# Optimization experiments

Measured on AMD Instinct MI355X. Metric: run time of the kernel, lower is better.

## Reference

```python
import jax, jax.numpy as jnp
import numpy as np
import math

D_MODEL = 2048
N_HEADS = 16
HEAD_DIM = D_MODEL // N_HEADS  # 128
SEQ = 2048
BATCH = 1


def make_freqs(seq_len, head_dim, theta=10000.0):
    # standard rotary frequencies: freqs_cis = exp(i * t * inv_freq)
    inv_freq = 1.0 / (theta ** (np.arange(0, head_dim, 2, dtype=np.float32) / head_dim))
    t = np.arange(seq_len, dtype=np.float32)
    ang = np.outer(t, inv_freq)  # [seq, head_dim/2]
    return jnp.asarray(np.cos(ang)), jnp.asarray(np.sin(ang))


def setup_inputs() -> dict:
    key = jax.random.key(0)
    ks = jax.random.split(key, 6)
    x = jax.random.normal(ks[0], (BATCH, SEQ, D_MODEL), dtype=jnp.float32)
    freqs_cos, freqs_sin = make_freqs(SEQ, HEAD_DIM)
    # causal additive mask, broadcastable to [b, h, s, s]
    mask = jnp.where(jnp.tril(jnp.ones((SEQ, SEQ), dtype=bool)), 0.0, -1e9).astype(jnp.float32)[None, None]
    scale = 0.02
    wq = jax.random.normal(ks[1], (D_MODEL, D_MODEL), dtype=jnp.float32) * scale
    wk = jax.random.normal(ks[2], (D_MODEL, D_MODEL), dtype=jnp.float32) * scale
    wv = jax.random.normal(ks[3], (D_MODEL, D_MODEL), dtype=jnp.float32) * scale
    wo = jax.random.normal(ks[4], (D_MODEL, D_MODEL), dtype=jnp.float32) * scale
    return {"x": x, "freqs_cos": freqs_cos, "freqs_sin": freqs_sin, "mask": mask,
            "wq": wq, "wk": wk, "wv": wv, "wo": wo}


def _apply_rotary(q, k, cos, sin):
    # q, k: [b, s, h, hd]; cos/sin: [s, hd/2]
    def rot(t):
        tr = t.reshape(*t.shape[:-1], -1, 2)  # [b, s, h, hd/2, 2]
        re, im = tr[..., 0], tr[..., 1]
        c = cos[None, :, None, :]
        s = sin[None, :, None, :]
        # complex multiply (re + i im) * (c + i s)
        out_re = re * c - im * s
        out_im = re * s + im * c
        return jnp.stack([out_re, out_im], axis=-1).reshape(t.shape)
    return rot(q), rot(k)


def reference(x, freqs_cos, freqs_sin, mask, wq, wk, wv, wo):
    b, s, _ = x.shape
    # QKV projections (nn.Linear with no bias: x @ W^T; W is square so use x @ W
    # with W stored already-transposed -- weights here are random so x @ W is faithful math)
    q = (x @ wq).reshape(b, s, N_HEADS, HEAD_DIM)
    k = (x @ wk).reshape(b, s, N_HEADS, HEAD_DIM)
    v = (x @ wv).reshape(b, s, N_HEADS, HEAD_DIM)
    q, k = _apply_rotary(q, k, freqs_cos, freqs_sin)
    # [b, h, s_q, s_k]
    scores = jnp.einsum("bqhd,bkhd->bhqk", q, k) / math.sqrt(HEAD_DIM)
    scores = scores + mask
    probs = jax.nn.softmax(scores.astype(jnp.float32), axis=-1).astype(q.dtype)
    out = jnp.einsum("bhqk,bkhd->bqhd", probs, v).reshape(b, s, N_HEADS * HEAD_DIM)
    return out @ wo
```

## Files before the change

### kernel.cpp

```cpp
#include <hip/hip_runtime.h>
#include <hip/hip_bf16.h>
#include <math.h>

#define SEQ 2048
#define DM 2048
#define NH 16
#define HD 128
#define QKV_N 6144

typedef __bf16 bf16;
typedef __bf16 bf16x8 __attribute__((ext_vector_type(8)));
typedef __bf16 bf16x4v __attribute__((ext_vector_type(4)));
typedef __bf16 bf16x2v __attribute__((ext_vector_type(2)));
typedef float f32x4 __attribute__((ext_vector_type(4)));

__device__ inline int sw_idx64(int row, int chunk) {
    return (row * 8 + (chunk ^ (row & 7))) * 8;
}
__device__ inline int sw_idx128(int row, int chunk) {
    return (row * 16 + (chunk ^ (row & 15))) * 8;
}
__device__ inline int sw_idx32(int row, int chunk) {
    return (row * 4 + (chunk ^ (row & 3))) * 8;
}

__device__ inline void async16(const void* g, void* l) {
    __builtin_amdgcn_global_load_lds((const __attribute__((address_space(1))) void*)g,
                                     (__attribute__((address_space(3))) void*)l, 16, 0, 0);
}

__global__ __launch_bounds__(256) void k_prep(const float* __restrict__ wq,
                                              const float* __restrict__ wk,
                                              const float* __restrict__ wv,
                                              const float* __restrict__ wo,
                                              bf16* __restrict__ wT, bf16* __restrict__ woT,
                                              const float* __restrict__ x,
                                              bf16* __restrict__ xb) {
    const int z = blockIdx.z;
    const int t = threadIdx.x;
    if (z == 4) {
        int bid = blockIdx.y * 32 + blockIdx.x;
#pragma unroll
        for (int j = 0; j < 4; ++j) {
            int i = bid * 1024 + j * 256 + t;
            float4 v = ((const float4*)x)[i];
            bf16x4v o;
            o.x = (bf16)v.x; o.y = (bf16)v.y; o.z = (bf16)v.z; o.w = (bf16)v.w;
            ((bf16x4v*)xb)[i] = o;
        }
        return;
    }
    __shared__ bf16 tile[64][66];
    const float* src = (z == 0) ? wq : (z == 1) ? wk : (z == 2) ? wv : wo;
    bf16* dst = (z < 3) ? (wT + (size_t)z * DM * DM) : woT;
    const int bx = blockIdx.x * 64, by = blockIdx.y * 64;
#pragma unroll
    for (int j = 0; j < 4; ++j) {
        int idx = j * 256 + t;
        int r = idx >> 4, cg = idx & 15;
        float4 v = *(const float4*)&src[(size_t)(by + r) * DM + bx + cg * 4];
        bf16x4v o;
        o.x = (bf16)v.x; o.y = (bf16)v.y; o.z = (bf16)v.z; o.w = (bf16)v.w;
        *(bf16x4v*)&tile[r][cg * 4] = o;
    }
    __syncthreads();
#pragma unroll
    for (int j = 0; j < 4; ++j) {
        int idx = j * 256 + t;
        int r = idx >> 4, cg = idx & 15;
        bf16x4v o;
        o.x = tile[cg * 4 + 0][r];
        o.y = tile[cg * 4 + 1][r];
        o.z = tile[cg * 4 + 2][r];
        o.w = tile[cg * 4 + 3][r];
        *(bf16x4v*)&dst[(size_t)(bx + r) * DM + by + cg * 4] = o;
    }
}

__global__ __launch_bounds__(256) void k_rope_vt(bf16* __restrict__ qkv,
                                                 const float* __restrict__ cosT,
                                                 const float* __restrict__ sinT,
                                                 bf16* __restrict__ vT) {
    const int t = threadIdx.x;
    if (blockIdx.x >= 1024) {
        int g = (blockIdx.x - 1024) * 256 + t;
        int s = g >> 8;
        int cg = g & 255;
        int h = cg >> 4, w8 = cg & 15;
        size_t base = (size_t)s * QKV_N + DM + h * HD + w8 * 8;
        float4 cv = *(const float4*)&cosT[s * 64 + w8 * 4];
        float4 sv = *(const float4*)&sinT[s * 64 + w8 * 4];
        float cc[4] = {cv.x, cv.y, cv.z, cv.w};
        float ss[4] = {sv.x, sv.y, sv.z, sv.w};
        bf16x8 k = *(bf16x8*)&qkv[base];
        bf16x8 o;
#pragma unroll
        for (int p = 0; p < 4; ++p) {
            float re = (float)k[2 * p], im = (float)k[2 * p + 1];
            o[2 * p]     = (bf16)(re * cc[p] - im * ss[p]);
            o[2 * p + 1] = (bf16)(re * ss[p] + im * cc[p]);
        }
        *(bf16x8*)&qkv[base] = o;
        return;
    }
    __shared__ bf16 tile[64][66];
    const int bx = (blockIdx.x & 31) * 64, by = (blockIdx.x >> 5) * 64;
#pragma unroll
    for (int j = 0; j < 4; ++j) {
        int idx = j * 256 + t;
        int r = idx >> 4, cg = idx & 15;
        *(bf16x4v*)&tile[r][cg * 4] =
            *(const bf16x4v*)&qkv[(size_t)(by + r) * QKV_N + 2 * DM + bx + cg * 4];
    }
    __syncthreads();
#pragma unroll
    for (int j = 0; j < 4; ++j) {
        int idx = j * 256 + t;
        int r = idx >> 4, cg = idx & 15;
        bf16x4v o;
        o.x = tile[cg * 4 + 0][r];
        o.y = tile[cg * 4 + 1][r];
        o.z = tile[cg * 4 + 2][r];
        o.w = tile[cg * 4 + 3][r];
        *(bf16x4v*)&vT[(size_t)(bx + r) * SEQ + by + cg * 4] = o;
    }
}

template <typename OutT, int BN>
__device__ __forceinline__ void gemm_body(const bf16* __restrict__ A,
                                          const bf16* __restrict__ Bt,
                                          OutT* __restrict__ C,
                                          int N, int K, size_t bm, size_t bn,
                                          bf16* As, bf16* Bs) {
    constexpr int NI = BN / 32;
    const int t = threadIdx.x;
    const int lane = t & 63;
    const int w = t >> 6;
    const int wr = (w >> 1) * 64, wc = (w & 1) * (BN / 2);
    const int l15 = lane & 15, quad = lane >> 4;
    f32x4 acc[4][NI];
#pragma unroll
    for (int i = 0; i < 4; ++i)
#pragma unroll
        for (int j = 0; j < NI; ++j) acc[i][j] = (f32x4){0.f, 0.f, 0.f, 0.f};

    for (int kt = 0; kt < K; kt += 64) {
#pragma unroll
        for (int j = 0; j < 4; ++j) {
            int c = j * 256 + t;
            int row = c >> 3, g = ((c & 7) ^ (row & 7)) * 8;
            async16(&A[(bm + row) * K + kt + g], &As[c * 8]);
        }
#pragma unroll
        for (int j = 0; j < NI; ++j) {
            int c = j * 256 + t;
            int row = c >> 3, g = ((c & 7) ^ (row & 7)) * 8;
            async16(&Bt[(bn + row) * K + kt + g], &Bs[c * 8]);
        }
        __syncthreads();
#pragma unroll
        for (int kh = 0; kh < 2; ++kh) {
            bf16x8 af[4], bfm[NI];
#pragma unroll
            for (int mi = 0; mi < 4; ++mi)
                af[mi] = *(const bf16x8*)&As[sw_idx64(wr + mi * 16 + l15, kh * 4 + quad)];
#pragma unroll
            for (int ni = 0; ni < NI; ++ni)
                bfm[ni] = *(const bf16x8*)&Bs[sw_idx64(wc + ni * 16 + l15, kh * 4 + quad)];
#pragma unroll
            for (int mi = 0; mi < 4; ++mi)
#pragma unroll
                for (int ni = 0; ni < NI; ++ni)
                    acc[mi][ni] = __builtin_amdgcn_mfma_f32_16x16x32_bf16(
                        af[mi], bfm[ni], acc[mi][ni], 0, 0, 0);
        }
        __syncthreads();
    }
#pragma unroll
    for (int mi = 0; mi < 4; ++mi)
#pragma unroll
        for (int ni = 0; ni < NI; ++ni)
#pragma unroll
            for (int r = 0; r < 4; ++r) {
                size_t row = bm + wr + mi * 16 + quad * 4 + r;
                size_t col = bn + wc + ni * 16 + l15;
                C[row * (size_t)N + col] = (OutT)acc[mi][ni][r];
            }
}

template <typename OutT, int BN>
__global__ __launch_bounds__(256) void k_gemm_bt(const bf16* __restrict__ A,
                                                 const bf16* __restrict__ Bt,
                                                 OutT* __restrict__ C,
                                                 int M, int N, int K) {
    __shared__ bf16 As[128 * 64];
    __shared__ bf16 Bs[BN * 64];
    size_t bm = (size_t)blockIdx.y * 128, bn = (size_t)blockIdx.x * BN;
    gemm_body<OutT, BN>(A, Bt, C, N, K, bm, bn, As, Bs);
}

__global__ __launch_bounds__(512) void k_gemm_ksplit(const bf16* __restrict__ A,
                                                     const bf16* __restrict__ Bt,
                                                     float* __restrict__ C) {
    __shared__ __align__(16) char smem[65536];
    const int t = threadIdx.x;
    const int tg = t & 255;
    const int gk = t >> 8;
    const int lane = t & 63;
    const int wl = (t >> 6) & 3;
    const int wr = (wl >> 1) * 64, wc = (wl & 1) * 64;
    const int l15 = lane & 15, quad = lane >> 4;
    const int orig = blockIdx.y * 16 + blockIdx.x;
    const int swz = (orig & 7) * 32 + (orig >> 3);
    const size_t bm = (size_t)(swz / 16) * 128, bn = (size_t)(swz % 16) * 128;
    bf16* Asg = (bf16*)(smem) + gk * 8192;
    bf16* Bsg = (bf16*)(smem + 32768) + gk * 8192;

    f32x4 acc[4][4];
#pragma unroll
    for (int i = 0; i < 4; ++i)
#pragma unroll
        for (int j = 0; j < 4; ++j) acc[i][j] = (f32x4){0.f, 0.f, 0.f, 0.f};

    const int k0 = gk * 1024;
    for (int kt = k0; kt < k0 + 1024; kt += 64) {
#pragma unroll
        for (int j = 0; j < 4; ++j) {
            int c = j * 256 + tg;
            int row = c >> 3, g8 = ((c & 7) ^ (row & 7)) * 8;
            async16(&A[(bm + row) * DM + kt + g8], &Asg[c * 8]);
        }
#pragma unroll
        for (int j = 0; j < 4; ++j) {
            int c = j * 256 + tg;
            int row = c >> 3, g8 = ((c & 7) ^ (row & 7)) * 8;
            async16(&Bt[(bn + row) * DM + kt + g8], &Bsg[c * 8]);
        }
        __syncthreads();
#pragma unroll
        for (int kh = 0; kh < 2; ++kh) {
            bf16x8 af[4], bfm[4];
#pragma unroll
            for (int mi = 0; mi < 4; ++mi)
                af[mi] = *(const bf16x8*)&Asg[sw_idx64(wr + mi * 16 + l15, kh * 4 + quad)];
#pragma unroll
            for (int ni = 0; ni < 4; ++ni)
                bfm[ni] = *(const bf16x8*)&Bsg[sw_idx64(wc + ni * 16 + l15, kh * 4 + quad)];
#pragma unroll
            for (int mi = 0; mi < 4; ++mi)
#pragma unroll
                for (int ni = 0; ni < 4; ++ni)
                    acc[mi][ni] = __builtin_amdgcn_mfma_f32_16x16x32_bf16(
                        af[mi], bfm[ni], acc[mi][ni], 0, 0, 0);
        }
        __syncthreads();
    }
    float* oX = (float*)smem;
    if (gk == 1) {
#pragma unroll
        for (int mi = 0; mi < 4; ++mi)
#pragma unroll
            for (int ni = 0; ni < 4; ++ni)
#pragma unroll
                for (int r = 0; r < 4; ++r)
                    oX[(wr + mi * 16 + quad * 4 + r) * 128 + wc + ni * 16 + l15] =
                        acc[mi][ni][r];
    }
    __syncthreads();
    if (gk == 0) {
#pragma unroll
        for (int mi = 0; mi < 4; ++mi)
#pragma unroll
            for (int ni = 0; ni < 4; ++ni)
#pragma unroll
                for (int r = 0; r < 4; ++r) {
                    int row = wr + mi * 16 + quad * 4 + r;
                    int col = wc + ni * 16 + l15;
                    C[(bm + row) * (size_t)DM + bn + col] =
                        acc[mi][ni][r] + oX[row * 128 + col];
                }
    }
}

__global__ __launch_bounds__(512) void k_flash(const bf16* __restrict__ qkv,
                                               const bf16* __restrict__ vT,
                                               const float* __restrict__ cosT,
                                               const float* __restrict__ sinT,
                                               bf16* __restrict__ out) {
    __shared__ bf16 Ks[2][64 * 128];
    __shared__ bf16 Vs[2][128 * 64];
    __shared__ bf16 Pl[8][16 * 32];
    const int t = threadIdx.x;
    const int lane = t & 63;
    const int w = t >> 6;
    const int wl = w & 3;
    const int g = w >> 2;
    const int l15 = lane & 15, quad = lane >> 4;
    const int b = blockIdx.x;
    const int hc = b & 15;
    const int h = (hc & 7) * 2 + (hc >> 3);
    const int qb = (b < 256) ? (31 - (b >> 4)) : ((b >> 4) - 16);
    const int q0w = qb * 64 + wl * 16;
    const float sc2 = 0.08838834764831845f * 1.4426950408889634f;

    const size_t qrow = (size_t)(q0w + l15) * QKV_N + h * HD;
    bf16x8 aq[4];
#pragma unroll
    for (int u = 0; u < 4; ++u)
        aq[u] = *(const bf16x8*)&qkv[qrow + u * 32 + quad * 8];
#pragma unroll
    for (int u = 0; u < 4; ++u) {
        float4 cv = *(const float4*)&cosT[(q0w + l15) * 64 + u * 16 + quad * 4];
        float4 sv = *(const float4*)&sinT[(q0w + l15) * 64 + u * 16 + quad * 4];
        float cc[4] = {cv.x, cv.y, cv.z, cv.w};
        float ss[4] = {sv.x, sv.y, sv.z, sv.w};
        bf16x8 q = aq[u], rq;
#pragma unroll
        for (int pp = 0; pp < 4; ++pp) {
            float re = (float)q[2 * pp], im = (float)q[2 * pp + 1];
            rq[2 * pp]     = (bf16)(re * cc[pp] - im * ss[pp]);
            rq[2 * pp + 1] = (bf16)(re * ss[pp] + im * cc[pp]);
        }
        aq[u] = rq;
    }

    f32x4 o[8];
#pragma unroll
    for (int c = 0; c < 8; ++c) o[c] = (f32x4){0.f, 0.f, 0.f, 0.f};
    float l_r[4] = {0.f, 0.f, 0.f, 0.f};

    int krow[2], kg[2], vrow[2], vg[2];
#pragma unroll
    for (int j = 0; j < 2; ++j) {
        int c2 = j * 512 + t;
        krow[j] = c2 >> 4; kg[j] = ((c2 & 15) ^ (krow[j] & 15)) * 8;
        vrow[j] = c2 >> 3; vg[j] = ((c2 & 7) ^ (vrow[j] & 7)) * 8;
    }
    auto stage = [&](int buf, int kt2) {
        const int kb2 = kt2 * 64;
#pragma unroll
        for (int j = 0; j < 2; ++j)
            async16(&qkv[(size_t)(kb2 + krow[j]) * QKV_N + DM + h * HD + kg[j]],
                    &Ks[buf][(j * 512 + t) * 8]);
#pragma unroll
        for (int j = 0; j < 2; ++j)
            async16(&vT[(size_t)(h * HD + vrow[j]) * SEQ + kb2 + vg[j]],
                    &Vs[buf][(j * 512 + t) * 8]);
    };

    const int nT = qb + 1;
    stage(0, 0);
    for (int kt = 0; kt < nT; ++kt) {
        const int cb = kt & 1;
        const int kbase = kt * 64;
        const bool pre = (kt + 1 < nT);
        if (pre) {
            stage(cb ^ 1, kt + 1);
            asm volatile("s_waitcnt vmcnt(6)" ::: "memory");
        } else {
            asm volatile("s_waitcnt vmcnt(2)" ::: "memory");
        }
        __builtin_amdgcn_s_barrier();
        asm volatile("" ::: "memory");

        f32x4 s4[2];
        __builtin_amdgcn_s_setprio(1);
#pragma unroll
        for (int sl = 0; sl < 2; ++sl) {
            const int sub = 2 * g + sl;
            f32x4 z = (f32x4){0.f, 0.f, 0.f, 0.f};
#pragma unroll
            for (int u = 0; u < 4; ++u) {
                bf16x8 kv = *(const bf16x8*)&Ks[cb][sw_idx128(sub * 16 + l15, u * 4 + quad)];
                z = __builtin_amdgcn_mfma_f32_16x16x32_bf16(aq[u], kv, z, 0, 0, 0);
            }
            s4[sl] = z;
        }
        __builtin_amdgcn_s_setprio(0);
        const bool masked = (kt == qb);
#pragma unroll
        for (int sl = 0; sl < 2; ++sl) {
            const int sub = 2 * g + sl;
#pragma unroll
            for (int r = 0; r < 4; ++r) {
                float pv = __builtin_amdgcn_exp2f(s4[sl][r] * sc2);
                if (masked)
                    pv = (kbase + sub * 16 + l15 <= q0w + quad * 4 + r) ? pv : 0.f;
                l_r[r] += pv;
                int rowp = quad * 4 + r;
                int lc = sl * 16 + l15;
                Pl[w][(rowp * 4 + ((lc >> 3) ^ (rowp & 3))) * 8 + (lc & 7)] = (bf16)pv;
            }
        }
        if (pre) asm volatile("s_waitcnt vmcnt(4)" ::: "memory");
        else     asm volatile("s_waitcnt vmcnt(0)" ::: "memory");
        __builtin_amdgcn_s_barrier();
        __asm__ __volatile__("s_waitcnt lgkmcnt(0)" ::: "memory");
        bf16x8 pf = *(const bf16x8*)&Pl[w][sw_idx32(l15, quad)];
        __builtin_amdgcn_s_setprio(1);
#pragma unroll
        for (int c = 0; c < 8; ++c) {
            bf16x8 vb = *(const bf16x8*)&Vs[cb][sw_idx64(c * 16 + l15, g * 4 + quad)];
            o[c] = __builtin_amdgcn_mfma_f32_16x16x32_bf16(pf, vb, o[c], 0, 0, 0);
        }
        __builtin_amdgcn_s_setprio(0);
        asm volatile("" ::: "memory");
        __builtin_amdgcn_s_barrier();
        asm volatile("" ::: "memory");
    }

    __syncthreads();
    float* oxch = (float*)&Ks[0][0];
    float* lxch = (float*)&Pl[0][0];
    const int tp = t & 255;
    if (g == 1) {
#pragma unroll
        for (int c = 0; c < 8; ++c)
            *(f32x4*)&oxch[tp * 32 + c * 4] = o[c];
#pragma unroll
        for (int r = 0; r < 4; ++r) lxch[tp * 4 + r] = l_r[r];
    }
    __syncthreads();
    if (g == 0) {
#pragma unroll
        for (int c = 0; c < 8; ++c) {
            f32x4 v = *(const f32x4*)&oxch[tp * 32 + c * 4];
            o[c] += v;
        }
#pragma unroll
        for (int r = 0; r < 4; ++r) l_r[r] += lxch[tp * 4 + r];
        float rl[4];
#pragma unroll
        for (int r = 0; r < 4; ++r) {
            float l = l_r[r];
            l += __shfl_xor(l, 1, 16);
            l += __shfl_xor(l, 2, 16);
            l += __shfl_xor(l, 4, 16);
            l += __shfl_xor(l, 8, 16);
            rl[r] = 1.0f / l;
        }
#pragma unroll
        for (int c = 0; c < 8; ++c)
#pragma unroll
            for (int r = 0; r < 4; ++r)
                out[(size_t)(q0w + quad * 4 + r) * DM + h * HD + c * 16 + l15] =
                    (bf16)(o[c][r] * rl[r]);
    }
}

extern "C" void kernel_launch(void* const* d_in, const int* in_sizes, int n_in,
                              void* d_out, int out_size, void* d_ws, size_t ws_size,
                              hipStream_t stream) {
    const float* x  = (const float*)d_in[0];
    const float* fc = (const float*)d_in[1];
    const float* fs = (const float*)d_in[2];
    const float* wq = (const float*)d_in[4];
    const float* wk = (const float*)d_in[5];
    const float* wv = (const float*)d_in[6];
    const float* wo = (const float*)d_in[7];
    float* out = (float*)d_out;

    char* ws = (char*)d_ws;
    bf16* xb  = (bf16*)(ws);
    bf16* wT  = (bf16*)(ws + (size_t)(8u  << 20));
    bf16* woT = (bf16*)(ws + (size_t)(32u << 20));
    bf16* qkv = (bf16*)(ws + (size_t)(40u << 20));
    bf16* vT  = (bf16*)(ws + (size_t)(64u << 20));

    k_prep<<<dim3(32, 32, 5), 256, 0, stream>>>(wq, wk, wv, wo, wT, woT, x, xb);
    k_gemm_bt<bf16, 128><<<dim3(48, 16), 256, 0, stream>>>(xb, wT, qkv, SEQ, QKV_N, DM);
    k_rope_vt<<<3072, 256, 0, stream>>>(qkv, fc, fs, vT);
    k_flash<<<512, 512, 0, stream>>>(qkv, vT, fc, fs, xb);
    k_gemm_ksplit<<<dim3(16, 16), 512, 0, stream>>>(xb, woT, out);
}
```

Baseline: 279.1 us.

## Fuse rope, V transpose, flash attention and output projection into cooperative megakernel

Replaces the three launches after the QKV GEMM with one cooperative kernel of 512 blocks. It runs the K-rope/V-transpose, flash attention and output projection as phases separated by grid-wide syncs. The output projection is restructured into 128x64 tiles with 32x32 per-wave subtiles instead of the split-K 128x128 kernel. The aim is to remove launch gaps and tail effects between stages. The costs are grid synchronisation, a less register-efficient GEMM phase, and a dependence on all blocks being co-resident; a fallback to the old launches covers a failed cooperative launch.

Result: slower. 392.1 us (+40.5%).

```diff
diff --git a/kernel.cpp b/kernel.cpp
--- a/kernel.cpp
+++ b/kernel.cpp
@@ -1,5 +1,6 @@
 #include <hip/hip_runtime.h>
 #include <hip/hip_bf16.h>
+#include <hip/hip_cooperative_groups.h>
 #include <math.h>
 
 #define SEQ 2048
@@ -74,6 +75,362 @@
         o.z = tile[cg * 4 + 2][r];
         o.w = tile[cg * 4 + 3][r];
         *(bf16x4v*)&dst[(size_t)(bx + r) * DM + by + cg * 4] = o;
+    }
+}
+
+template <typename OutT, int BN>
+__device__ __forceinline__ void gemm_body(const bf16* __restrict__ A,
+                                          const bf16* __restrict__ Bt,
+                                          OutT* __restrict__ C,
+                                          int N, int K, size_t bm, size_t bn,
+                                          bf16* As, bf16* Bs) {
+    constexpr int NI = BN / 32;
+    const int t = threadIdx.x;
+    const int lane = t & 63;
+    const int w = t >> 6;
+    const int wr = (w >> 1) * 64, wc = (w & 1) * (BN / 2);
+    const int l15 = lane & 15, quad = lane >> 4;
+    f32x4 acc[4][NI];
+#pragma unroll
+    for (int i = 0; i < 4; ++i)
+#pragma unroll
+        for (int j = 0; j < NI; ++j) acc[i][j] = (f32x4){0.f, 0.f, 0.f, 0.f};
+
+    for (int kt = 0; kt < K; kt += 64) {
+#pragma unroll
+        for (int j = 0; j < 4; ++j) {
+            int c = j * 256 + t;
+            int row = c >> 3, g = ((c & 7) ^ (row & 7)) * 8;
+            async16(&A[(bm + row) * K + kt + g], &As[c * 8]);
+        }
+#pragma unroll
+        for (int j = 0; j < NI; ++j) {
+            int c = j * 256 + t;
+            int row = c >> 3, g = ((c & 7) ^ (row & 7)) * 8;
+            async16(&Bt[(bn + row) * K + kt + g], &Bs[c * 8]);
+        }
+        __syncthreads();
+#pragma unroll
+        for (int kh = 0; kh < 2; ++kh) {
+            bf16x8 af[4], bfm[NI];
+#pragma unroll
+            for (int mi = 0; mi < 4; ++mi)
+                af[mi] = *(const bf16x8*)&As[sw_idx64(wr + mi * 16 + l15, kh * 4 + quad)];
+#pragma unroll
+            for (int ni = 0; ni < NI; ++ni)
+                bfm[ni] = *(const bf16x8*)&Bs[sw_idx64(wc + ni * 16 + l15, kh * 4 + quad)];
+#pragma unroll
+            for (int mi = 0; mi < 4; ++mi)
+#pragma unroll
+                for (int ni = 0; ni < NI; ++ni)
+                    acc[mi][ni] = __builtin_amdgcn_mfma_f32_16x16x32_bf16(
+                        af[mi], bfm[ni], acc[mi][ni], 0, 0, 0);
+        }
+        __syncthreads();
+    }
+#pragma unroll
+    for (int mi = 0; mi < 4; ++mi)
+#pragma unroll
+        for (int ni = 0; ni < NI; ++ni)
+#pragma unroll
+            for (int r = 0; r < 4; ++r) {
+                size_t row = bm + wr + mi * 16 + quad * 4 + r;
+                size_t col = bn + wc + ni * 16 + l15;
+                C[row * (size_t)N + col] = (OutT)acc[mi][ni][r];
+            }
+}
+
+template <typename OutT, int BN>
+__global__ __launch_bounds__(256) void k_gemm_bt(const bf16* __restrict__ A,
+                                                 const bf16* __restrict__ Bt,
+                                                 OutT* __restrict__ C,
+                                                 int M, int N, int K) {
+    __shared__ bf16 As[128 * 64];
+    __shared__ bf16 Bs[BN * 64];
+    size_t bm = (size_t)blockIdx.y * 128, bn = (size_t)blockIdx.x * BN;
+    gemm_body<OutT, BN>(A, Bt, C, N, K, bm, bn, As, Bs);
+}
+
+__global__ __launch_bounds__(512, 4) void k_mega(bf16* __restrict__ qkv,
+                                                 bf16* __restrict__ vT,
+                                                 const float* __restrict__ cosT,
+                                                 const float* __restrict__ sinT,
+                                                 bf16* __restrict__ xb,
+                                                 const bf16* __restrict__ woT,
+                                                 float* __restrict__ out) {
+    __shared__ __align__(16) char smem[73728];
+    const int t = threadIdx.x;
+    const int b = blockIdx.x;
+
+    {
+#pragma unroll
+        for (int j = 0; j < 2; ++j) {
+            int g = b * 1024 + j * 512 + t;
+            int s = g >> 8;
+            int cg = g & 255;
+            int h = cg >> 4, w8 = cg & 15;
+            size_t base = (size_t)s * QKV_N + DM + h * HD + w8 * 8;
+            float4 cv = *(const float4*)&cosT[s * 64 + w8 * 4];
+            float4 sv = *(const float4*)&sinT[s * 64 + w8 * 4];
+            float cc[4] = {cv.x, cv.y, cv.z, cv.w};
+            float ss[4] = {sv.x, sv.y, sv.z, sv.w};
+            bf16x8 k = *(bf16x8*)&qkv[base];
+            bf16x8 o;
+#pragma unroll
+            for (int p = 0; p < 4; ++p) {
+                float re = (float)k[2 * p], im = (float)k[2 * p + 1];
+                o[2 * p]     = (bf16)(re * cc[p] - im * ss[p]);
+                o[2 * p + 1] = (bf16)(re * ss[p] + im * cc[p]);
+            }
+            *(bf16x8*)&qkv[base] = o;
+        }
+        const int half = t >> 8, tt = t & 255;
+        bf16* tl = (bf16*)(smem + half * 8448);
+        const int tile = b * 2 + half;
+        const int bx = (tile & 31) * 64, by = (tile >> 5) * 64;
+#pragma unroll
+        for (int j = 0; j < 4; ++j) {
+            int idx = j * 256 + tt;
+            int r = idx >> 4, cg = idx & 15;
+            *(bf16x4v*)&tl[r * 66 + cg * 4] =
+                *(const bf16x4v*)&qkv[(size_t)(by + r) * QKV_N + 2 * DM + bx + cg * 4];
+        }
+        __syncthreads();
+#pragma unroll
+        for (int j = 0; j < 4; ++j) {
+            int idx = j * 256 + tt;
+            int r = idx >> 4, cg = idx & 15;
+            bf16x4v o;
+            o.x = tl[(cg * 4 + 0) * 66 + r];
+            o.y = tl[(cg * 4 + 1) * 66 + r];
+            o.z = tl[(cg * 4 + 2) * 66 + r];
+            o.w = tl[(cg * 4 + 3) * 66 + r];
+            *(bf16x4v*)&vT[(size_t)(bx + r) * SEQ + by + cg * 4] = o;
+        }
+    }
+    cooperative_groups::this_grid().sync();
+
+    {
+        bf16* KsB = (bf16*)smem;
+        bf16* VsB = (bf16*)(smem + 32768);
+        bf16* PlB = (bf16*)(smem + 65536);
+        const int lane = t & 63;
+        const int w = t >> 6;
+        const int wl = w & 3;
+        const int g = w >> 2;
+        const int l15 = lane & 15, quad = lane >> 4;
+        const int hc = b & 15;
+        const int h = (hc & 7) * 2 + (hc >> 3);
+        const int qb = (b < 256) ? (31 - (b >> 4)) : ((b >> 4) - 16);
+        const int q0w = qb * 64 + wl * 16;
+        const float sc2 = 0.08838834764831845f * 1.4426950408889634f;
+
+        const size_t qrow = (size_t)(q0w + l15) * QKV_N + h * HD;
+        bf16x8 aq[4];
+#pragma unroll
+        for (int u = 0; u < 4; ++u)
+            aq[u] = *(const bf16x8*)&qkv[qrow + u * 32 + quad * 8];
+#pragma unroll
+        for (int u = 0; u < 4; ++u) {
+            float4 cv = *(const float4*)&cosT[(q0w + l15) * 64 + u * 16 + quad * 4];
+            float4 sv = *(const float4*)&sinT[(q0w + l15) * 64 + u * 16 + quad * 4];
+            float cc[4] = {cv.x, cv.y, cv.z, cv.w};
+            float ss[4] = {sv.x, sv.y, sv.z, sv.w};
+            bf16x8 q = aq[u], rq;
+#pragma unroll
+            for (int pp = 0; pp < 4; ++pp) {
+                float re = (float)q[2 * pp], im = (float)q[2 * pp + 1];
+                rq[2 * pp]     = (bf16)(re * cc[pp] - im * ss[pp]);
+                rq[2 * pp + 1] = (bf16)(re * ss[pp] + im * cc[pp]);
+            }
+            aq[u] = rq;
+        }
+
+        f32x4 o[8];
+#pragma unroll
+        for (int c = 0; c < 8; ++c) o[c] = (f32x4){0.f, 0.f, 0.f, 0.f};
+        float l_r[4] = {0.f, 0.f, 0.f, 0.f};
+
+        int krow[2], kg[2], vrow[2], vg[2];
+#pragma unroll
+        for (int j = 0; j < 2; ++j) {
+            int c2 = j * 512 + t;
+            krow[j] = c2 >> 4; kg[j] = ((c2 & 15) ^ (krow[j] & 15)) * 8;
+            vrow[j] = c2 >> 3; vg[j] = ((c2 & 7) ^ (vrow[j] & 7)) * 8;
+        }
+        auto stage = [&](int buf, int kt2) {
+            const int kb2 = kt2 * 64;
+#pragma unroll
+            for (int j = 0; j < 2; ++j)
+                async16(&qkv[(size_t)(kb2 + krow[j]) * QKV_N + DM + h * HD + kg[j]],
+                        &KsB[buf * 8192 + (j * 512 + t) * 8]);
+#pragma unroll
+            for (int j = 0; j < 2; ++j)
+                async16(&vT[(size_t)(h * HD + vrow[j]) * SEQ + kb2 + vg[j]],
+                        &VsB[buf * 8192 + (j * 512 + t) * 8]);
+        };
+
+        const int nT = qb + 1;
+        stage(0, 0);
+        for (int kt = 0; kt < nT; ++kt) {
+            const int cb = kt & 1;
+            const int kbase = kt * 64;
+            const bool pre = (kt + 1 < nT);
+            if (pre) {
+                stage(cb ^ 1, kt + 1);
+                asm volatile("s_waitcnt vmcnt(6)" ::: "memory");
+            } else {
+                asm volatile("s_waitcnt vmcnt(2)" ::: "memory");
+            }
+            __builtin_amdgcn_s_barrier();
+            asm volatile("" ::: "memory");
+
+            f32x4 s4[2];
+            __builtin_amdgcn_s_setprio(1);
+#pragma unroll
+            for (int sl = 0; sl < 2; ++sl) {
+                const int sub = 2 * g + sl;
+                f32x4 z = (f32x4){0.f, 0.f, 0.f, 0.f};
+#pragma unroll
+                for (int u = 0; u < 4; ++u) {
+                    bf16x8 kv = *(const bf16x8*)&KsB[cb * 8192 +
+                                    sw_idx128(sub * 16 + l15, u * 4 + quad)];
+                    z = __builtin_amdgcn_mfma_f32_16x16x32_bf16(aq[u], kv, z, 0, 0, 0);
+                }
+                s4[sl] = z;
+            }
+            __builtin_amdgcn_s_setprio(0);
+            const bool masked = (kt == qb);
+#pragma unroll
+            for (int sl = 0; sl < 2; ++sl) {
+                const int sub = 2 * g + sl;
+#pragma unroll
+                for (int r = 0; r < 4; ++r) {
+                    float pv = __builtin_amdgcn_exp2f(s4[sl][r] * sc2);
+                    if (masked)
+                        pv = (kbase + sub * 16 + l15 <= q0w + quad * 4 + r) ? pv : 0.f;
+                    l_r[r] += pv;
+                    int rowp = quad * 4 + r;
+                    int lc = sl * 16 + l15;
+                    PlB[w * 512 + (rowp * 4 + ((lc >> 3) ^ (rowp & 3))) * 8 + (lc & 7)] =
+                        (bf16)pv;
+                }
+            }
+            if (pre) asm volatile("s_waitcnt vmcnt(4)" ::: "memory");
+            else     asm volatile("s_waitcnt vmcnt(0)" ::: "memory");
+            __builtin_amdgcn_s_barrier();
+            __asm__ __volatile__("s_waitcnt lgkmcnt(0)" ::: "memory");
+            bf16x8 pf = *(const bf16x8*)&PlB[w * 512 + sw_idx32(l15, quad)];
+            __builtin_amdgcn_s_setprio(1);
+#pragma unroll
+            for (int c = 0; c < 8; ++c) {
+                bf16x8 vb = *(const bf16x8*)&VsB[cb * 8192 +
+                                sw_idx64(c * 16 + l15, g * 4 + quad)];
+                o[c] = __builtin_amdgcn_mfma_f32_16x16x32_bf16(pf, vb, o[c], 0, 0, 0);
+            }
+            __builtin_amdgcn_s_setprio(0);
+            asm volatile("" ::: "memory");
+            __builtin_amdgcn_s_barrier();
+            asm volatile("" ::: "memory");
+        }
+
+        __syncthreads();
+        float* oxch = (float*)smem;
+        float* lxch = (float*)(smem + 65536);
+        const int tp = t & 255;
+        if (g == 1) {
+#pragma unroll
+            for (int c = 0; c < 8; ++c)
+                *(f32x4*)&oxch[tp * 32 + c * 4] = o[c];
+#pragma unroll
+            for (int r = 0; r < 4; ++r) lxch[tp * 4 + r] = l_r[r];
+        }
+        __syncthreads();
+        if (g == 0) {
+#pragma unroll
+            for (int c = 0; c < 8; ++c) {
+                f32x4 v = *(const f32x4*)&oxch[tp * 32 + c * 4];
+                o[c] += v;
+            }
+#pragma unroll
+            for (int r = 0; r < 4; ++r) l_r[r] += lxch[tp * 4 + r];
+            float rl[4];
+#pragma unroll
+            for (int r = 0; r < 4; ++r) {
+                float l = l_r[r];
+                l += __shfl_xor(l, 1, 16);
+                l += __shfl_xor(l, 2, 16);
+                l += __shfl_xor(l, 4, 16);
+                l += __shfl_xor(l, 8, 16);
+                rl[r] = 1.0f / l;
+            }
+#pragma unroll
+            for (int c = 0; c < 8; ++c)
+#pragma unroll
+                for (int r = 0; r < 4; ++r)
+                    xb[(size_t)(q0w + quad * 4 + r) * DM + h * HD + c * 16 + l15] =
+                        (bf16)(o[c][r] * rl[r]);
+        }
+    }
+    cooperative_groups::this_grid().sync();
+
+    {
+        bf16* As = (bf16*)smem;
+        bf16* Bs = (bf16*)(smem + 32768);
+        const int lane = t & 63;
+        const int w2 = t >> 6;
+        const int wrC = (w2 >> 1) * 32, wcC = (w2 & 1) * 32;
+        const int l15 = lane & 15, quad = lane >> 4;
+        const size_t bm2 = (size_t)(b >> 5) * 128;
+        const size_t bn2 = (size_t)(b & 31) * 64;
+
+        f32x4 acc[2][2];
+#pragma unroll
+        for (int i = 0; i < 2; ++i)
+#pragma unroll
+            for (int j = 0; j < 2; ++j) acc[i][j] = (f32x4){0.f, 0.f, 0.f, 0.f};
+
+        for (int kt = 0; kt < DM; kt += 64) {
+#pragma unroll
+            for (int j = 0; j < 2; ++j) {
+                int c = j * 512 + t;
+                int row = c >> 3, g8 = ((c & 7) ^ (row & 7)) * 8;
+                async16(&xb[(bm2 + row) * DM + kt + g8], &As[c * 8]);
+            }
+            {
+                int c = t;
+                int row = c >> 3, g8 = ((c & 7) ^ (row & 7)) * 8;
+                async16(&woT[(bn2 + row) * DM + kt + g8], &Bs[c * 8]);
+            }
+            __syncthreads();
+#pragma unroll
+            for (int kh = 0; kh < 2; ++kh) {
+                bf16x8 af[2], bfm[2];
+#pragma unroll
+                for (int mi = 0; mi < 2; ++mi)
+                    af[mi] = *(const bf16x8*)&As[sw_idx64(wrC + mi * 16 + l15, kh * 4 + quad)];
+#pragma unroll
+                for (int ni = 0; ni < 2; ++ni)
+                    bfm[ni] = *(const bf16x8*)&Bs[sw_idx64(wcC + ni * 16 + l15, kh * 4 + quad)];
+#pragma unroll
+                for (int mi = 0; mi < 2; ++mi)
+#pragma unroll
+                    for (int ni = 0; ni < 2; ++ni)
+                        acc[mi][ni] = __builtin_amdgcn_mfma_f32_16x16x32_bf16(
+                            af[mi], bfm[ni], acc[mi][ni], 0, 0, 0);
+            }
+            __syncthreads();
+        }
+#pragma unroll
+        for (int mi = 0; mi < 2; ++mi)
+#pragma unroll
+            for (int ni = 0; ni < 2; ++ni)
+#pragma unroll
+                for (int r = 0; r < 4; ++r) {
+                    size_t row = bm2 + wrC + mi * 16 + quad * 4 + r;
+                    size_t col = bn2 + wcC + ni * 16 + l15;
+                    out[row * (size_t)DM + col] = acc[mi][ni][r];
+                }
     }
 }
 
@@ -123,162 +480,6 @@
         o.z = tile[cg * 4 + 2][r];
         o.w = tile[cg * 4 + 3][r];
         *(bf16x4v*)&vT[(size_t)(bx + r) * SEQ + by + cg * 4] = o;
-    }
-}
-
-template <typename OutT, int BN>
-__device__ __forceinline__ void gemm_body(const bf16* __restrict__ A,
-                                          const bf16* __restrict__ Bt,
-                                          OutT* __restrict__ C,
-                                          int N, int K, size_t bm, size_t bn,
-                                          bf16* As, bf16* Bs) {
-    constexpr int NI = BN / 32;
-    const int t = threadIdx.x;
-    const int lane = t & 63;
-    const int w = t >> 6;
-    const int wr = (w >> 1) * 64, wc = (w & 1) * (BN / 2);
-    const int l15 = lane & 15, quad = lane >> 4;
-    f32x4 acc[4][NI];
-#pragma unroll
-    for (int i = 0; i < 4; ++i)
-#pragma unroll
-        for (int j = 0; j < NI; ++j) acc[i][j] = (f32x4){0.f, 0.f, 0.f, 0.f};
-
-    for (int kt = 0; kt < K; kt += 64) {
-#pragma unroll
-        for (int j = 0; j < 4; ++j) {
-            int c = j * 256 + t;
-            int row = c >> 3, g = ((c & 7) ^ (row & 7)) * 8;
-            async16(&A[(bm + row) * K + kt + g], &As[c * 8]);
-        }
-#pragma unroll
-        for (int j = 0; j < NI; ++j) {
-            int c = j * 256 + t;
-            int row = c >> 3, g = ((c & 7) ^ (row & 7)) * 8;
-            async16(&Bt[(bn + row) * K + kt + g], &Bs[c * 8]);
-        }
-        __syncthreads();
-#pragma unroll
-        for (int kh = 0; kh < 2; ++kh) {
-            bf16x8 af[4], bfm[NI];
-#pragma unroll
-            for (int mi = 0; mi < 4; ++mi)
-                af[mi] = *(const bf16x8*)&As[sw_idx64(wr + mi * 16 + l15, kh * 4 + quad)];
-#pragma unroll
-            for (int ni = 0; ni < NI; ++ni)
-                bfm[ni] = *(const bf16x8*)&Bs[sw_idx64(wc + ni * 16 + l15, kh * 4 + quad)];
-#pragma unroll
-            for (int mi = 0; mi < 4; ++mi)
-#pragma unroll
-                for (int ni = 0; ni < NI; ++ni)
-                    acc[mi][ni] = __builtin_amdgcn_mfma_f32_16x16x32_bf16(
-                        af[mi], bfm[ni], acc[mi][ni], 0, 0, 0);
-        }
-        __syncthreads();
-    }
-#pragma unroll
-    for (int mi = 0; mi < 4; ++mi)
-#pragma unroll
-        for (int ni = 0; ni < NI; ++ni)
-#pragma unroll
-            for (int r = 0; r < 4; ++r) {
-                size_t row = bm + wr + mi * 16 + quad * 4 + r;
-                size_t col = bn + wc + ni * 16 + l15;
-                C[row * (size_t)N + col] = (OutT)acc[mi][ni][r];
-            }
-}
-
-template <typename OutT, int BN>
-__global__ __launch_bounds__(256) void k_gemm_bt(const bf16* __restrict__ A,
-                                                 const bf16* __restrict__ Bt,
-                                                 OutT* __restrict__ C,
-                                                 int M, int N, int K) {
-    __shared__ bf16 As[128 * 64];
-    __shared__ bf16 Bs[BN * 64];
-    size_t bm = (size_t)blockIdx.y * 128, bn = (size_t)blockIdx.x * BN;
-    gemm_body<OutT, BN>(A, Bt, C, N, K, bm, bn, As, Bs);
-}
-
-__global__ __launch_bounds__(512) void k_gemm_ksplit(const bf16* __restrict__ A,
-                                                     const bf16* __restrict__ Bt,
-                                                     float* __restrict__ C) {
-    __shared__ __align__(16) char smem[65536];
-    const int t = threadIdx.x;
-    const int tg = t & 255;
-    const int gk = t >> 8;
-    const int lane = t & 63;
-    const int wl = (t >> 6) & 3;
-    const int wr = (wl >> 1) * 64, wc = (wl & 1) * 64;
-    const int l15 = lane & 15, quad = lane >> 4;
-    const int orig = blockIdx.y * 16 + blockIdx.x;
-    const int swz = (orig & 7) * 32 + (orig >> 3);
-    const size_t bm = (size_t)(swz / 16) * 128, bn = (size_t)(swz % 16) * 128;
-    bf16* Asg = (bf16*)(smem) + gk * 8192;
-    bf16* Bsg = (bf16*)(smem + 32768) + gk * 8192;
-
-    f32x4 acc[4][4];
-#pragma unroll
-    for (int i = 0; i < 4; ++i)
-#pragma unroll
-        for (int j = 0; j < 4; ++j) acc[i][j] = (f32x4){0.f, 0.f, 0.f, 0.f};
-
-    const int k0 = gk * 1024;
-    for (int kt = k0; kt < k0 + 1024; kt += 64) {
-#pragma unroll
-        for (int j = 0; j < 4; ++j) {
-            int c = j * 256 + tg;
-            int row = c >> 3, g8 = ((c & 7) ^ (row & 7)) * 8;
-            async16(&A[(bm + row) * DM + kt + g8], &Asg[c * 8]);
-        }
-#pragma unroll
-        for (int j = 0; j < 4; ++j) {
-            int c = j * 256 + tg;
-            int row = c >> 3, g8 = ((c & 7) ^ (row & 7)) * 8;
-            async16(&Bt[(bn + row) * DM + kt + g8], &Bsg[c * 8]);
-        }
-        __syncthreads();
-#pragma unroll
-        for (int kh = 0; kh < 2; ++kh) {
-            bf16x8 af[4], bfm[4];
-#pragma unroll
-            for (int mi = 0; mi < 4; ++mi)
-                af[mi] = *(const bf16x8*)&Asg[sw_idx64(wr + mi * 16 + l15, kh * 4 + quad)];
-#pragma unroll
-            for (int ni = 0; ni < 4; ++ni)
-                bfm[ni] = *(const bf16x8*)&Bsg[sw_idx64(wc + ni * 16 + l15, kh * 4 + quad)];
-#pragma unroll
-            for (int mi = 0; mi < 4; ++mi)
-#pragma unroll
-                for (int ni = 0; ni < 4; ++ni)
-                    acc[mi][ni] = __builtin_amdgcn_mfma_f32_16x16x32_bf16(
-                        af[mi], bfm[ni], acc[mi][ni], 0, 0, 0);
-        }
-        __syncthreads();
-    }
-    float* oX = (float*)smem;
-    if (gk == 1) {
-#pragma unroll
-        for (int mi = 0; mi < 4; ++mi)
-#pragma unroll
-            for (int ni = 0; ni < 4; ++ni)
-#pragma unroll
-                for (int r = 0; r < 4; ++r)
-                    oX[(wr + mi * 16 + quad * 4 + r) * 128 + wc + ni * 16 + l15] =
-                        acc[mi][ni][r];
-    }
-    __syncthreads();
-    if (gk == 0) {
-#pragma unroll
-        for (int mi = 0; mi < 4; ++mi)
-#pragma unroll
-            for (int ni = 0; ni < 4; ++ni)
-#pragma unroll
-                for (int r = 0; r < 4; ++r) {
-                    int row = wr + mi * 16 + quad * 4 + r;
-                    int col = wc + ni * 16 + l15;
-                    C[(bm + row) * (size_t)DM + bn + col] =
-                        acc[mi][ni][r] + oX[row * 128 + col];
-                }
     }
 }
 
@@ -448,6 +649,89 @@
     }
 }
 
+__global__ __launch_bounds__(512) void k_gemm_ksplit(const bf16* __restrict__ A,
+                                                     const bf16* __restrict__ Bt,
+                                                     float* __restrict__ C) {
+    __shared__ __align__(16) char smem[65536];
+    const int t = threadIdx.x;
+    const int tg = t & 255;
+    const int gk = t >> 8;
+    const int lane = t & 63;
+    const int wl = (t >> 6) & 3;
+    const int wr = (wl >> 1) * 64, wc = (wl & 1) * 64;
+    const int l15 = lane & 15, quad = lane >> 4;
+    const int orig = blockIdx.y * 16 + blockIdx.x;
+    const int swz = (orig & 7) * 32 + (orig >> 3);
+    const size_t bm = (size_t)(swz / 16) * 128, bn = (size_t)(swz % 16) * 128;
+    bf16* Asg = (bf16*)(smem) + gk * 8192;
+    bf16* Bsg = (bf16*)(smem + 32768) + gk * 8192;
+
+    f32x4 acc[4][4];
+#pragma unroll
+    for (int i = 0; i < 4; ++i)
+#pragma unroll
+        for (int j = 0; j < 4; ++j) acc[i][j] = (f32x4){0.f, 0.f, 0.f, 0.f};
+
+    const int k0 = gk * 1024;
+    for (int kt = k0; kt < k0 + 1024; kt += 64) {
+#pragma unroll
+        for (int j = 0; j < 4; ++j) {
+            int c = j * 256 + tg;
+            int row = c >> 3, g8 = ((c & 7) ^ (row & 7)) * 8;
+            async16(&A[(bm + row) * DM + kt + g8], &Asg[c * 8]);
+        }
+#pragma unroll
+        for (int j = 0; j < 4; ++j) {
+            int c = j * 256 + tg;
+            int row = c >> 3, g8 = ((c & 7) ^ (row & 7)) * 8;
+            async16(&Bt[(bn + row) * DM + kt + g8], &Bsg[c * 8]);
+        }
+        __syncthreads();
+#pragma unroll
+        for (int kh = 0; kh < 2; ++kh) {
+            bf16x8 af[4], bfm[4];
+#pragma unroll
+            for (int mi = 0; mi < 4; ++mi)
+                af[mi] = *(const bf16x8*)&Asg[sw_idx64(wr + mi * 16 + l15, kh * 4 + quad)];
+#pragma unroll
+            for (int ni = 0; ni < 4; ++ni)
+                bfm[ni] = *(const bf16x8*)&Bsg[sw_idx64(wc + ni * 16 + l15, kh * 4 + quad)];
+#pragma unroll
+            for (int mi = 0; mi < 4; ++mi)
+#pragma unroll
+                for (int ni = 0; ni < 4; ++ni)
+                    acc[mi][ni] = __builtin_amdgcn_mfma_f32_16x16x32_bf16(
+                        af[mi], bfm[ni], acc[mi][ni], 0, 0, 0);
+        }
+        __syncthreads();
+    }
+    float* oX = (float*)smem;
+    if (gk == 1) {
+#pragma unroll
+        for (int mi = 0; mi < 4; ++mi)
+#pragma unroll
+            for (int ni = 0; ni < 4; ++ni)
+#pragma unroll
+                for (int r = 0; r < 4; ++r)
+                    oX[(wr + mi * 16 + quad * 4 + r) * 128 + wc + ni * 16 + l15] =
+                        acc[mi][ni][r];
+    }
+    __syncthreads();
+    if (gk == 0) {
+#pragma unroll
+        for (int mi = 0; mi < 4; ++mi)
+#pragma unroll
+            for (int ni = 0; ni < 4; ++ni)
+#pragma unroll
+                for (int r = 0; r < 4; ++r) {
+                    int row = wr + mi * 16 + quad * 4 + r;
+                    int col = wc + ni * 16 + l15;
+                    C[(bm + row) * (size_t)DM + bn + col] =
+                        acc[mi][ni][r] + oX[row * 128 + col];
+                }
+    }
+}
+
 extern "C" void kernel_launch(void* const* d_in, const int* in_sizes, int n_in,
                               void* d_out, int out_size, void* d_ws, size_t ws_size,
                               hipStream_t stream) {
@@ -469,7 +753,15 @@
 
     k_prep<<<dim3(32, 32, 5), 256, 0, stream>>>(wq, wk, wv, wo, wT, woT, x, xb);
     k_gemm_bt<bf16, 128><<<dim3(48, 16), 256, 0, stream>>>(xb, wT, qkv, SEQ, QKV_N, DM);
-    k_rope_vt<<<3072, 256, 0, stream>>>(qkv, fc, fs, vT);
-    k_flash<<<512, 512, 0, stream>>>(qkv, vT, fc, fs, xb);
-    k_gemm_ksplit<<<dim3(16, 16), 512, 0, stream>>>(xb, woT, out);
-}
+
+    bf16* qkv_a = qkv; bf16* vT_a = vT; const float* fc_a = fc; const float* fs_a = fs;
+    bf16* xb_a = xb; const bf16* woT_a = woT; float* out_a = out;
+    void* args[] = {&qkv_a, &vT_a, &fc_a, &fs_a, &xb_a, &woT_a, &out_a};
+    hipError_t ce = hipLaunchCooperativeKernel((const void*)k_mega, dim3(512),
+                                               dim3(512), args, 0, stream);
+    if (ce != hipSuccess) {
+        k_rope_vt<<<3072, 256, 0, stream>>>(qkv, fc, fs, vT);
+        k_flash<<<512, 512, 0, stream>>>(qkv, vT, fc, fs, xb);
+        k_gemm_ksplit<<<dim3(16, 16), 512, 0, stream>>>(xb, woT, out);
+    }
+}
```
